# Performance work log

Measured on AMD Instinct MI355X. Metric: run time of the kernel, lower is better.

Reference implementation:

```python
import jax, jax.numpy as jnp
import numpy as np

N = 100_000      # nodes
E_HALF = 1_600_000  # undirected edges (mirrored -> 3.2M directed)
D = 128          # feature dim
K = 1            # k-MIS hop parameter


def setup_inputs() -> dict:
    key = jax.random.key(0)
    k1, k2, k3, k4, k5 = jax.random.split(key, 5)
    x = jax.random.normal(k1, (N, D), dtype=jnp.float32)
    src = jax.random.randint(k2, (E_HALF,), 0, N)
    dst = jax.random.randint(k3, (E_HALF,), 0, N)
    # symmetric edge list (undirected graph), as k-MIS coverage assumes
    edge_index = jnp.stack([jnp.concatenate([src, dst]),
                            jnp.concatenate([dst, src])])
    ea = jax.random.uniform(k4, (E_HALF,), dtype=jnp.float32)
    edge_attr = jnp.concatenate([ea, ea])
    # RandomScorer: score is a uniform random vector over nodes
    score = jax.random.uniform(k5, (N,), dtype=jnp.float32)
    return {"x": x, "edge_index": edge_index, "edge_attr": edge_attr, "score": score}


def _scatter_min(values, index, n, fill):
    return jnp.full((n,), fill, dtype=values.dtype).at[index].min(values)


def maximal_k_independent_set(row, col, n, k, rank):
    # Iteratively: propagate min rank k hops; nodes equal to their own
    # (uncovered) min rank join the MIS; mark their k-hop neighborhood covered.
    mis = jnp.zeros(n, dtype=bool)
    mask = jnp.zeros(n, dtype=bool)
    min_rank = rank
    while not bool(mask.all()):
        for _ in range(k):
            mn = _scatter_min(min_rank[row], col, n, n)
            min_rank = jnp.minimum(mn, min_rank)
        mis = mis | ((rank == min_rank) & ~mask)
        mask = mask | mis
        for _ in range(k):
            nb = jnp.zeros(n, dtype=bool).at[col].max(mask[row])
            mask = mask | nb
        min_rank = jnp.where(mask, n, rank)
    return mis


def cluster_k_mis(mis, row, col, n, k, rank):
    # assign every node to the MIS node of minimum rank within k hops
    min_rank = jnp.where(mis, rank, n)
    for _ in range(k):
        mn = _scatter_min(min_rank[row], col, n, n)
        min_rank = jnp.minimum(mn, min_rank)
    _, clusters = jnp.unique(min_rank, return_inverse=True)  # sorted uniques
    perm = jnp.argsort(rank[mis])  # sorted-rank position -> index into x[mis]
    return perm[clusters.ravel()]


def reference(x, edge_index, edge_attr, score):
    n = x.shape[0]
    row, col = edge_index[0], edge_index[1]
    # Greedy ordering: rank = inverse permutation of argsort(score)
    rank = jnp.argsort(jnp.argsort(score))
    mis = maximal_k_independent_set(row, col, n, K, rank)
    cluster = cluster_k_mis(mis, row, col, n, K, rank)
    # sparse_reduce_adj: map edges into cluster space, coalesce with sum
    pairs = jnp.stack([cluster[row], cluster[col]], axis=1)  # [E,2]
    uk, inv = jnp.unique(pairs, axis=0, return_inverse=True)
    vals = jax.ops.segment_sum(edge_attr, inv.ravel(), num_segments=uk.shape[0])
    r2, c2 = uk[:, 0], uk[:, 1]
    keep = r2 != c2  # remove_self_loops
    edge_index_out = jnp.stack([r2[keep], c2[keep]])
    edge_attr_out = vals[keep]
    x_out = x[jnp.nonzero(mis)[0]]  # reduce_x=None -> select MIS node features
    return x_out, edge_index_out, edge_attr_out, cluster, mis, score
```

## Files before the change

kernel.cpp:

```cpp
#include <hip/hip_runtime.h>
#include <stdint.h>

#define RTILE 4096
#define ROUNDS 12


__global__ void k_init_counters(int* counters){
  int t = threadIdx.x;
  counters[t] = 0;
  if (t == 7) counters[7] = 1;
}
__global__ void k_init_nodes(int* mis, int N){
  int v = blockIdx.x*blockDim.x + threadIdx.x;
  if (v < N) mis[v]=0;
}
__global__ void k_zero_vals(float* vals, int E){
  int i = blockIdx.x*blockDim.x + threadIdx.x;
  if (i < E) vals[i]=0.f;
}

__global__ void k_score_key(const float* score, unsigned* keys, unsigned* pay, int N){
  int i = blockIdx.x*blockDim.x+threadIdx.x;
  if (i<N){
    unsigned b = __float_as_uint(score[i]);
    b ^= ((int)b < 0) ? 0xFFFFFFFFu : 0x80000000u;
    keys[i]=b; pay[i]=(unsigned)i;
  }
}
__global__ void k_rank_build(const unsigned* pay, int* rank, int* pm, int N){
  int p = blockIdx.x*blockDim.x+threadIdx.x;
  if (p<N){ int v = (int)pay[p]; rank[v]=p; pm[v]=p; }
}
__global__ void k_make_colrow(const int* __restrict__ row, const int* __restrict__ col,
                              unsigned* __restrict__ keys, unsigned* __restrict__ pay, int E){
  int e = blockIdx.x*blockDim.x+threadIdx.x;
  if (e<E){ keys[e]=(unsigned)col[e]; pay[e]=(unsigned)row[e]; }
}

template<typename K, int TILE>
__global__ void k_radix_hist(const K* __restrict__ keys, int n, int shift,
                             unsigned* __restrict__ ghist, int numBlocks, const int* gate){
  if (*gate==0) return;
  __shared__ unsigned h[512];
  int t=threadIdx.x, b=blockIdx.x;
  h[t]=0; h[t+256]=0; __syncthreads();
  int base = b*TILE;
  for (int j=t; j<TILE; j+=256){
    int i = base+j;
    if (i<n){
      unsigned d = (unsigned)((keys[i]>>shift)&(K)511);
      atomicAdd(&h[d],1u);
    }
  }
  __syncthreads();
  ghist[(size_t)t*numBlocks + b] = h[t];
  ghist[(size_t)(t+256)*numBlocks + b] = h[t+256];
}

template<typename K, int TILE>
__global__ void k_radix_scatter(const K* __restrict__ keysIn, const unsigned* __restrict__ payIn,
                                K* __restrict__ keysOut, unsigned* __restrict__ payOut,
                                int n, int shift, const unsigned* __restrict__ gbase,
                                int numBlocks, const int* gate){
  int t=threadIdx.x, b=blockIdx.x;
  int base = b*TILE;
  if (*gate==0){
    for (int j=t; j<TILE; j+=256){
      int i = base+j;
      if (i<n){ keysOut[i]=keysIn[i]; payOut[i]=payIn[i]; }
    }
    return;
  }
  __shared__ unsigned carry[512];
  carry[t]=0; carry[t+256]=0; __syncthreads();
  int lane = t&63, wave = t>>6;
  for (int r=0; r<TILE/256; ++r){
    int i = base + r*256 + t;
    bool valid = i<n;
    K k = valid ? keysIn[i] : (K)0;
    unsigned pay = valid ? payIn[i] : 0u;
    unsigned d = (unsigned)((k>>shift)&(K)511);
    unsigned off=0;
    for (int w=0; w<4; ++w){
      if (wave==w){
        unsigned long long m = __ballot(valid);
        #pragma unroll
        for (int bit=0; bit<9; ++bit){
          unsigned long long bb = __ballot((d>>bit)&1u);
          m &= ((d>>bit)&1u) ? bb : ~bb;
        }
        int lr = __popcll(m & ((1ull<<lane)-1ull));
        unsigned cb = carry[d];
        off = cb + (unsigned)lr;
        if (valid && lr==0) carry[d] = cb + (unsigned)__popcll(m);
      }
      __syncthreads();
    }
    if (valid){
      unsigned pos = gbase[(size_t)d*numBlocks + b] + off;
      keysOut[pos]=k; payOut[pos]=pay;
    }
  }
}

__global__ void k_scan_single(unsigned* data, int n, unsigned* total, const int* gate){
  if (*gate==0) return;
  __shared__ unsigned sh[1024];
  __shared__ unsigned carry;
  int t=threadIdx.x;
  if (t==0) carry=0;
  __syncthreads();
  for (int base=0; base<n; base+=4096){
    unsigned v[4]; unsigned s=0;
    int i0 = base + t*4;
    #pragma unroll
    for (int j=0;j<4;j++){ int i=i0+j; v[j] = (i<n)?data[i]:0u; s+=v[j]; }
    sh[t]=s; __syncthreads();
    for (int off=1; off<1024; off<<=1){
      unsigned x = (t>=off)? sh[t-off]:0u; __syncthreads();
      sh[t]+=x; __syncthreads();
    }
    unsigned excl = (t?sh[t-1]:0u) + carry;
    #pragma unroll
    for (int j=0;j<4;j++){ int i=i0+j; if(i<n){ unsigned o=v[j]; data[i]=excl; excl+=o; } }
    unsigned tot = sh[1023];
    __syncthreads();
    if (t==0) carry += tot;
    __syncthreads();
  }
  if (total && t==0) *total = carry;
}

__global__ void k_scan_partials(const unsigned* __restrict__ in, unsigned* __restrict__ bsums,
                                int n, const int* gate){
  if (*gate==0) return;
  __shared__ unsigned sh[256];
  int b=blockIdx.x, t=threadIdx.x;
  long base = (long)b*RTILE + (long)t*16;
  unsigned s=0;
  #pragma unroll
  for (int j=0;j<16;j++){ long i=base+j; if(i<n) s+=in[i]; }
  sh[t]=s; __syncthreads();
  for (int off=128; off>0; off>>=1){ if(t<off) sh[t]+=sh[t+off]; __syncthreads(); }
  if (t==0) bsums[b]=sh[0];
}
__global__ void k_scan_final(const unsigned* __restrict__ in, unsigned* __restrict__ out,
                             const unsigned* __restrict__ bsums, int n, const int* gate){
  if (*gate==0) return;
  __shared__ unsigned sh[256];
  int b=blockIdx.x, t=threadIdx.x;
  long base = (long)b*RTILE + (long)t*16;
  unsigned v[16]; unsigned s=0;
  #pragma unroll
  for (int j=0;j<16;j++){ long i=base+j; v[j]=(i<n)?in[i]:0u; s+=v[j]; }
  sh[t]=s; __syncthreads();
  for (int off=1; off<256; off<<=1){
    unsigned x=(t>=off)?sh[t-off]:0u; __syncthreads(); sh[t]+=x; __syncthreads();
  }
  unsigned run=(t?sh[t-1]:0u)+bsums[b];
  #pragma unroll
  for (int j=0;j<16;j++){ long i=base+j; if(i<n){ unsigned o=v[j]; out[i]=run; run+=o; } }
}

__global__ void k_build_off(const unsigned* __restrict__ scol, int* __restrict__ off, int E, int N){
  int i = blockIdx.x*blockDim.x+threadIdx.x;
  if (i>=E) return;
  int c = (int)scol[i];
  int p = (i==0) ? -1 : (int)scol[i-1];
  for (int v=p+1; v<=c; ++v) off[v]=i;
  if (i==E-1){ for (int v=c+1; v<=N; ++v) off[v]=E; }
}

__global__ void k_round1(const int* __restrict__ off, const int* __restrict__ nbr,
                         const int* __restrict__ pm, int* __restrict__ mis,
                         int* __restrict__ maskA, int N, const int* gate){
  if (*gate==0) return;
  int v = blockIdx.x*blockDim.x+threadIdx.x;
  if (v>=N) return;
  int p = pm[v];
  if (p == N){ maskA[v]=1; return; }
  int m = p;
  int s=off[v], e=off[v+1];
  for (int j=s; j<e; ++j){ int u=nbr[j]; m = min(m, pm[u]); }
  int nm = (m == p);
  if (nm) mis[v]=1;
  maskA[v] = nm;
}
__global__ void k_round2(const int* __restrict__ off, const int* __restrict__ nbr,
                         const int* __restrict__ maskA, int* __restrict__ pm,
                         int N, int* cnt, const int* gate){
  if (*gate==0) return;
  int v = blockIdx.x*blockDim.x+threadIdx.x;
  int um = 0;
  if (v<N){
    int mk = maskA[v];
    int s=off[v], e=off[v+1];
    for (int j=s; j<e && !mk; ++j) mk |= maskA[nbr[j]];
    if (mk) pm[v] = N;
    um = !mk;
  }
  unsigned long long bm = __ballot(um);
  if ((threadIdx.x&63)==0 && bm) atomicAdd(cnt, (int)__popcll(bm));
}

__global__ void k_cl_init(const int* rank, const int* mis, int* pm, int N){
  int v = blockIdx.x*blockDim.x+threadIdx.x;
  if (v<N) pm[v] = mis[v] ? rank[v] : N;
}
__global__ void k_cl_gather(const int* __restrict__ off, const int* __restrict__ nbr,
                            const int* __restrict__ pm, int* __restrict__ mn, int N){
  int v = blockIdx.x*blockDim.x+threadIdx.x;
  if (v>=N) return;
  int m = pm[v];
  int s=off[v], e=off[v+1];
  for (int j=s; j<e; ++j) m = min(m, pm[nbr[j]]);
  mn[v] = m;
}
__global__ void k_copy_u32(const int* in, unsigned* out, int N){
  int v = blockIdx.x*blockDim.x+threadIdx.x;
  if (v<N) out[v]=(unsigned)in[v];
}
__global__ void k_cl_map(const int* rank, const int* mis, const unsigned* cidx,
                         int* map, int* rmax, int N){
  int v = blockIdx.x*blockDim.x+threadIdx.x;
  if (v<N && mis[v]){ map[rank[v]] = (int)cidx[v]; atomicMax(rmax, rank[v]); }
}
__global__ void k_cl_cluster(const int* mn, const int* map, const int* rmax, int* cluster, int N){
  int v = blockIdx.x*blockDim.x+threadIdx.x;
  if (v<N){
    int mr = mn[v];
    if (mr >= N) mr = *rmax;
    cluster[v] = map[mr];
  }
}
__global__ void k_gather_x(const float4* __restrict__ x, float4* __restrict__ out,
                           const int* __restrict__ mis, const unsigned* __restrict__ cidx,
                           int N, int D4){
  int t = blockIdx.x*blockDim.x+threadIdx.x;
  int v = t / D4, q = t - v*D4;
  if (v<N && mis[v]) out[(size_t)cidx[v]*D4 + q] = x[(size_t)v*D4 + q];
}

__global__ void k_set_gates(int* counters){
  int M = counters[1];
  int sh = (M<=1) ? 1 : (32-__clz((unsigned)(M-1)));
  int kb = 2*sh;
  counters[36] = sh;
  counters[32] = 1;
  counters[33] = (9  < kb);
  counters[34] = (18 < kb);
  counters[35] = (27 < kb);
}
__global__ void k_pair_key(const int* __restrict__ row, const int* __restrict__ col,
                           const int* __restrict__ cluster, const float* __restrict__ attr,
                           unsigned long long* __restrict__ keys, unsigned* __restrict__ pay,
                           const int* __restrict__ counters, int E){
  int e = blockIdx.x*blockDim.x+threadIdx.x;
  if (e<E){
    int sh = counters[36];
    unsigned a = (unsigned)cluster[row[e]], b=(unsigned)cluster[col[e]];
    keys[e] = ((unsigned long long)a<<sh) | b;
    pay[e] = __float_as_uint(attr[e]);
  }
}
__global__ void k_flags(const unsigned long long* __restrict__ keys,
                        unsigned* __restrict__ fhead, unsigned* __restrict__ fkeep,
                        const int* __restrict__ counters, int E){
  int i = blockIdx.x*blockDim.x+threadIdx.x;
  if (i<E){
    int sh = counters[36];
    unsigned long long k = keys[i];
    unsigned head = (i==0) || (k != keys[i-1]);
    unsigned a=(unsigned)(k>>sh), b=(unsigned)(k & ((1ull<<sh)-1ull));
    fhead[i]=head;
    fkeep[i]=(head && a!=b) ? 1u : 0u;
  }
}
__global__ void k_acc_seg(const unsigned long long* __restrict__ keys,
                          const unsigned* __restrict__ pay,
                          const unsigned* __restrict__ excl1,
                          float* __restrict__ vals, int E){
  int i = blockIdx.x*blockDim.x+threadIdx.x;
  int lane = threadIdx.x & 63;
  bool valid = i < E;
  unsigned long long k = valid ? keys[i] : ~0ull;
  float v = valid ? __uint_as_float(pay[i]) : 0.f;
  #pragma unroll
  for (int off=1; off<64; off<<=1){
    float o = __shfl_up(v, off);
    unsigned long long ko = __shfl_up(k, off);
    if (lane >= off && ko == k) v += o;
  }
  if (valid){
    unsigned long long knext = (i+1<E) ? keys[i+1] : ~0ull;
    if (lane==63 || k != knext){
      unsigned head = (i==0) || (keys[i-1] != k);
      atomicAdd(&vals[excl1[i] + head - 1u], v);
    }
  }
}
__global__ void k_write_edges(const unsigned long long* __restrict__ keys,
                              const unsigned* __restrict__ excl1, const unsigned* __restrict__ excl2,
                              const float* __restrict__ vals, float* __restrict__ out,
                              const int* __restrict__ counters, int E, int D){
  int i = blockIdx.x*blockDim.x+threadIdx.x;
  if (i<E){
    int sh = counters[36];
    int head=(i==0)||(keys[i]!=keys[i-1]);
    unsigned a=(unsigned)(keys[i]>>sh), b=(unsigned)(keys[i] & ((1ull<<sh)-1ull));
    if (head && a!=b){
      unsigned opos = excl2[i];
      int M = counters[1], Ep = counters[3];
      size_t off = (size_t)M*D;
      out[off + opos] = (float)a;
      out[off + (size_t)Ep + opos] = (float)b;
      out[off + 2*(size_t)Ep + opos] = vals[excl1[i]];
    }
  }
}
__global__ void k_write_nodes(const int* __restrict__ cluster, const int* __restrict__ mis,
                              const float* __restrict__ score, float* __restrict__ out,
                              const int* __restrict__ counters, int N, int D){
  int v = blockIdx.x*blockDim.x+threadIdx.x;
  if (v<N){
    int M=counters[1], Ep=counters[3];
    size_t off = (size_t)M*D + 3*(size_t)Ep;
    out[off + v] = (float)cluster[v];
    out[off + (size_t)N + v] = mis[v] ? 1.f : 0.f;
    out[off + 2*(size_t)N + v] = score[v];
  }
}

extern "C" void kernel_launch(void* const* d_in, const int* in_sizes, int n_in,
                              void* d_out, int out_size, void* d_ws, size_t ws_size,
                              hipStream_t stream){
  const float* x     = (const float*)d_in[0];
  const int*   ei    = (const int*)d_in[1];
  const float* attr  = (const float*)d_in[2];
  const float* score = (const float*)d_in[3];
  int N = in_sizes[3];
  int E = in_sizes[2];
  int D = in_sizes[0]/N;
  const int* row = ei;
  const int* col = ei + E;
  float* out = (float*)d_out;

  char* p = (char*)d_ws;
  auto alloc = [&](size_t bytes)->char*{ char* r=p; p += ((bytes+255)/256)*256; return r; };
  unsigned long long* keyA = (unsigned long long*)alloc((size_t)E*8);
  unsigned long long* keyB = (unsigned long long*)alloc((size_t)E*8);
  unsigned* payA  = (unsigned*)alloc((size_t)E*4);
  unsigned* payB  = (unsigned*)alloc((size_t)E*4);
  unsigned* scanA = (unsigned*)alloc((size_t)E*4);
  unsigned* scanB = (unsigned*)alloc((size_t)E*4);
  float*    vals  = (float*)alloc((size_t)E*4);
  int* csr_row = (int*)alloc((size_t)E*4);
  int* off     = (int*)alloc((size_t)(N+1)*4);
  int* rank   = (int*)alloc((size_t)N*4);
  int* pm     = (int*)alloc((size_t)N*4);
  int* mis    = (int*)alloc((size_t)N*4);
  int* maskA  = (int*)alloc((size_t)N*4);
  int* mnArr  = (int*)alloc((size_t)N*4);
  int* map    = (int*)alloc((size_t)N*4);
  unsigned* cidx = (unsigned*)alloc((size_t)N*4);
  int* cluster= (int*)alloc((size_t)N*4);
  int* counters=(int*)alloc(256*4);
  int Be = (E + RTILE-1)/RTILE;
  int Bn1k = (N + 1023)/1024;
  unsigned* ghist = (unsigned*)alloc((size_t)512*Be*4);
  unsigned* bsums = (unsigned*)alloc(4096*4);

  int nbN = (N+255)/256, nbE = (E+255)/256;
  const int* ON = counters+7;

  auto big_scan = [&](unsigned* data, int n, unsigned* total, const int* gate){
    int B = (n + RTILE-1)/RTILE;
    k_scan_partials<<<B,256,0,stream>>>(data,bsums,n,gate);
    k_scan_single<<<1,1024,0,stream>>>(bsums,B,total,gate);
    k_scan_final<<<B,256,0,stream>>>(data,data,bsums,n,gate);
  };

  k_init_counters<<<1,256,0,stream>>>(counters);
  k_init_nodes<<<nbN,256,0,stream>>>(mis,N);
  k_zero_vals<<<nbE,256,0,stream>>>(vals,E);

  k_make_colrow<<<nbE,256,0,stream>>>(row,col,(unsigned*)keyA,payA,E);
  k_radix_hist<unsigned,RTILE><<<Be,256,0,stream>>>((unsigned*)keyA,E,0,ghist,Be,ON);
  big_scan(ghist,512*Be,nullptr,ON);
  k_radix_scatter<unsigned,RTILE><<<Be,256,0,stream>>>((unsigned*)keyA,payA,(unsigned*)keyB,payB,E,0,ghist,Be,ON);
  k_radix_hist<unsigned,RTILE><<<Be,256,0,stream>>>((unsigned*)keyB,E,9,ghist,Be,ON);
  big_scan(ghist,512*Be,nullptr,ON);
  k_radix_scatter<unsigned,RTILE><<<Be,256,0,stream>>>((unsigned*)keyB,payB,scanA,(unsigned*)csr_row,E,9,ghist,Be,ON);
  k_build_off<<<nbE,256,0,stream>>>(scanA,off,E,N);

  k_score_key<<<nbN,256,0,stream>>>(score,(unsigned*)keyA,payA,N);
  {
    unsigned *ki=(unsigned*)keyA,*ko=(unsigned*)keyB,*pi=payA,*po=payB;
    for (int pass=0; pass<4; ++pass){
      int shift = pass*9;
      k_radix_hist<unsigned,1024><<<Bn1k,256,0,stream>>>(ki,N,shift,ghist,Bn1k,ON);
      big_scan(ghist,512*Bn1k,nullptr,ON);
      k_radix_scatter<unsigned,1024><<<Bn1k,256,0,stream>>>(ki,pi,ko,po,N,shift,ghist,Bn1k,ON);
      unsigned* tk=ki; ki=ko; ko=tk; unsigned* tp=pi; pi=po; po=tp;
    }
    k_rank_build<<<nbN,256,0,stream>>>(pi, rank, pm, N);
  }

  for (int r=0; r<ROUNDS; ++r){
    const int* gate = (r==0) ? ON : (counters + 8 + r - 1);
    int* cnt = counters + 8 + r;
    k_round1<<<nbN,256,0,stream>>>(off,csr_row,pm,mis,maskA,N,gate);
    k_round2<<<nbN,256,0,stream>>>(off,csr_row,maskA,pm,N,cnt,gate);
  }

  k_cl_init<<<nbN,256,0,stream>>>(rank,mis,pm,N);
  k_cl_gather<<<nbN,256,0,stream>>>(off,csr_row,pm,mnArr,N);
  k_copy_u32<<<nbN,256,0,stream>>>(mis,cidx,N);
  big_scan(cidx,N,(unsigned*)(counters+1),ON);
  k_cl_map<<<nbN,256,0,stream>>>(rank,mis,cidx,map,counters+4,N);
  k_cl_cluster<<<nbN,256,0,stream>>>(mnArr,map,counters+4,cluster,N);
  k_gather_x<<<(N*(D/4)+255)/256,256,0,stream>>>((const float4*)x,(float4*)out,mis,cidx,N,D/4);

  k_set_gates<<<1,1,0,stream>>>(counters);
  k_pair_key<<<nbE,256,0,stream>>>(row,col,cluster,attr,keyA,payA,counters,E);
  {
    unsigned long long *ki=keyA,*ko=keyB; unsigned *pi=payA,*po=payB;
    for (int pass=0; pass<4; ++pass){
      int shift = pass*9;
      const int* g = counters + 32 + pass;
      k_radix_hist<unsigned long long,RTILE><<<Be,256,0,stream>>>(ki,E,shift,ghist,Be,g);
      big_scan(ghist,512*Be,nullptr,g);
      k_radix_scatter<unsigned long long,RTILE><<<Be,256,0,stream>>>(ki,pi,ko,po,E,shift,ghist,Be,g);
      unsigned long long* tk=ki; ki=ko; ko=tk; unsigned* tp=pi; pi=po; po=tp;
    }
    k_flags<<<nbE,256,0,stream>>>(keyA,scanA,scanB,counters,E);
    big_scan(scanA,E,(unsigned*)(counters+2),ON);
    big_scan(scanB,E,(unsigned*)(counters+3),ON);
    k_acc_seg<<<nbE,256,0,stream>>>(keyA,payA,scanA,vals,E);
    k_write_edges<<<nbE,256,0,stream>>>(keyA,scanA,scanB,vals,out,counters,E,D);
  }
  k_write_nodes<<<nbN,256,0,stream>>>(cluster,mis,score,out,counters,N,D);
}
```

Before: 1.094 ms.

## Build CSR with atomics, stage radix scatter in LDS, skip gated copies

Replaces the two-pass radix sort used to build the CSR with an atomic count, scan and atomic fill. The radix scatter is rewritten to compute local offsets, stage keys in shared memory and write coalesced to global memory. Gated-off passes now return early instead of copying, with a parity flag selecting the final buffer. The MIS round cap drops from 12 to 10, which risks an incomplete MIS if more rounds are needed, and the larger shared-memory footprint may lower occupancy.

```diff
diff --git a/kernel.cpp b/kernel.cpp
--- a/kernel.cpp
+++ b/kernel.cpp
@@ -2,7 +2,7 @@
 #include <stdint.h>
 
 #define RTILE 4096
-#define ROUNDS 12
+#define ROUNDS 10
 
 
 __global__ void k_init_counters(int* counters){
@@ -10,9 +10,10 @@
   counters[t] = 0;
   if (t == 7) counters[7] = 1;
 }
-__global__ void k_init_nodes(int* mis, int N){
+__global__ void k_init_nodes(int* mis, int* cur, int* cnt, int N){
   int v = blockIdx.x*blockDim.x + threadIdx.x;
-  if (v < N) mis[v]=0;
+  if (v < N){ mis[v]=0; cur[v]=0; }
+  if (v <= N) cnt[v]=0;
 }
 __global__ void k_zero_vals(float* vals, int E){
   int i = blockIdx.x*blockDim.x + threadIdx.x;
@@ -31,10 +32,20 @@
   int p = blockIdx.x*blockDim.x+threadIdx.x;
   if (p<N){ int v = (int)pay[p]; rank[v]=p; pm[v]=p; }
 }
-__global__ void k_make_colrow(const int* __restrict__ row, const int* __restrict__ col,
-                              unsigned* __restrict__ keys, unsigned* __restrict__ pay, int E){
+
+__global__ void k_csr_count(const int* __restrict__ col, int* __restrict__ cnt, int E){
   int e = blockIdx.x*blockDim.x+threadIdx.x;
-  if (e<E){ keys[e]=(unsigned)col[e]; pay[e]=(unsigned)row[e]; }
+  if (e<E) atomicAdd(&cnt[col[e]], 1);
+}
+__global__ void k_csr_fill(const int* __restrict__ row, const int* __restrict__ col,
+                           const unsigned* __restrict__ off, int* __restrict__ cur,
+                           int* __restrict__ csr_row, int E){
+  int e = blockIdx.x*blockDim.x+threadIdx.x;
+  if (e<E){
+    int c = col[e];
+    int p = atomicAdd(&cur[c], 1);
+    csr_row[off[c] + p] = row[e];
+  }
 }
 
 template<typename K, int TILE>
@@ -62,20 +73,38 @@
                                 K* __restrict__ keysOut, unsigned* __restrict__ payOut,
                                 int n, int shift, const unsigned* __restrict__ gbase,
                                 int numBlocks, const int* gate){
+  if (*gate==0) return;
+  __shared__ unsigned lbase[512];
+  __shared__ unsigned carry[512];
+  __shared__ unsigned ss[256];
+  __shared__ K        skey[TILE];
+  __shared__ unsigned spay[TILE];
   int t=threadIdx.x, b=blockIdx.x;
   int base = b*TILE;
-  if (*gate==0){
-    for (int j=t; j<TILE; j+=256){
-      int i = base+j;
-      if (i<n){ keysOut[i]=keysIn[i]; payOut[i]=payIn[i]; }
-    }
-    return;
-  }
-  __shared__ unsigned carry[512];
+  int cnt = min(TILE, n-base);
   carry[t]=0; carry[t+256]=0; __syncthreads();
+  for (int c=0;c<TILE/256;++c){
+    int i = base+c*256+t;
+    if (i<n){
+      unsigned d = (unsigned)((keysIn[i]>>shift)&(K)511);
+      atomicAdd(&carry[d],1u);
+    }
+  }
+  __syncthreads();
+  unsigned a0=carry[2*t], a1=carry[2*t+1];
+  ss[t]=a0+a1; __syncthreads();
+  for (int off=1; off<256; off<<=1){
+    unsigned x = (t>=off)? ss[t-off]:0u; __syncthreads();
+    ss[t]+=x; __syncthreads();
+  }
+  unsigned excl = t? ss[t-1]:0u;
+  __syncthreads();
+  lbase[2*t]=excl;      lbase[2*t+1]=excl+a0;
+  carry[2*t]=excl;      carry[2*t+1]=excl+a0;
+  __syncthreads();
   int lane = t&63, wave = t>>6;
-  for (int r=0; r<TILE/256; ++r){
-    int i = base + r*256 + t;
+  for (int c=0;c<TILE/256;++c){
+    int i = base + c*256 + t;
     bool valid = i<n;
     K k = valid ? keysIn[i] : (K)0;
     unsigned pay = valid ? payIn[i] : 0u;
@@ -96,9 +125,16 @@
       }
       __syncthreads();
     }
-    if (valid){
-      unsigned pos = gbase[(size_t)d*numBlocks + b] + off;
-      keysOut[pos]=k; payOut[pos]=pay;
+    if (valid){ skey[off]=k; spay[off]=pay; }
+  }
+  __syncthreads();
+  for (int c=0;c<TILE/256;++c){
+    int j = c*256 + t;
+    if (j<cnt){
+      K k = skey[j];
+      unsigned d = (unsigned)((k>>shift)&(K)511);
+      unsigned gpos = gbase[(size_t)d*numBlocks + b] + ((unsigned)j - lbase[d]);
+      keysOut[gpos]=k; payOut[gpos]=spay[j];
     }
   }
 }
@@ -162,15 +198,6 @@
   for (int j=0;j<16;j++){ long i=base+j; if(i<n){ unsigned o=v[j]; out[i]=run; run+=o; } }
 }
 
-__global__ void k_build_off(const unsigned* __restrict__ scol, int* __restrict__ off, int E, int N){
-  int i = blockIdx.x*blockDim.x+threadIdx.x;
-  if (i>=E) return;
-  int c = (int)scol[i];
-  int p = (i==0) ? -1 : (int)scol[i-1];
-  for (int v=p+1; v<=c; ++v) off[v]=i;
-  if (i==E-1){ for (int v=c+1; v<=N; ++v) off[v]=E; }
-}
-
 __global__ void k_round1(const int* __restrict__ off, const int* __restrict__ nbr,
                          const int* __restrict__ pm, int* __restrict__ mis,
                          int* __restrict__ maskA, int N, const int* gate){
@@ -245,11 +272,13 @@
   int M = counters[1];
   int sh = (M<=1) ? 1 : (32-__clz((unsigned)(M-1)));
   int kb = 2*sh;
+  int npass = 1 + (9<kb) + (18<kb) + (27<kb);
   counters[36] = sh;
   counters[32] = 1;
   counters[33] = (9  < kb);
   counters[34] = (18 < kb);
   counters[35] = (27 < kb);
+  counters[37] = npass & 1;
 }
 __global__ void k_pair_key(const int* __restrict__ row, const int* __restrict__ col,
                            const int* __restrict__ cluster, const float* __restrict__ attr,
@@ -263,9 +292,11 @@
     pay[e] = __float_as_uint(attr[e]);
   }
 }
-__global__ void k_flags(const unsigned long long* __restrict__ keys,
+__global__ void k_flags(const unsigned long long* __restrict__ keyA,
+                        const unsigned long long* __restrict__ keyB,
                         unsigned* __restrict__ fhead, unsigned* __restrict__ fkeep,
                         const int* __restrict__ counters, int E){
+  const unsigned long long* keys = counters[37] ? keyB : keyA;
   int i = blockIdx.x*blockDim.x+threadIdx.x;
   if (i<E){
     int sh = counters[36];
@@ -276,10 +307,13 @@
     fkeep[i]=(head && a!=b) ? 1u : 0u;
   }
 }
-__global__ void k_acc_seg(const unsigned long long* __restrict__ keys,
-                          const unsigned* __restrict__ pay,
+__global__ void k_acc_seg(const unsigned long long* __restrict__ keyA,
+                          const unsigned long long* __restrict__ keyB,
+                          const unsigned* __restrict__ payA, const unsigned* __restrict__ payB,
                           const unsigned* __restrict__ excl1,
-                          float* __restrict__ vals, int E){
+                          float* __restrict__ vals, const int* __restrict__ counters, int E){
+  const unsigned long long* keys = counters[37] ? keyB : keyA;
+  const unsigned* pay = counters[37] ? payB : payA;
   int i = blockIdx.x*blockDim.x+threadIdx.x;
   int lane = threadIdx.x & 63;
   bool valid = i < E;
@@ -299,10 +333,12 @@
     }
   }
 }
-__global__ void k_write_edges(const unsigned long long* __restrict__ keys,
+__global__ void k_write_edges(const unsigned long long* __restrict__ keyA,
+                              const unsigned long long* __restrict__ keyB,
                               const unsigned* __restrict__ excl1, const unsigned* __restrict__ excl2,
                               const float* __restrict__ vals, float* __restrict__ out,
                               const int* __restrict__ counters, int E, int D){
+  const unsigned long long* keys = counters[37] ? keyB : keyA;
   int i = blockIdx.x*blockDim.x+threadIdx.x;
   if (i<E){
     int sh = counters[36];
@@ -355,7 +391,8 @@
   unsigned* scanB = (unsigned*)alloc((size_t)E*4);
   float*    vals  = (float*)alloc((size_t)E*4);
   int* csr_row = (int*)alloc((size_t)E*4);
-  int* off     = (int*)alloc((size_t)(N+1)*4);
+  unsigned* off= (unsigned*)alloc((size_t)(N+1)*4);
+  int* cur     = (int*)alloc((size_t)N*4);
   int* rank   = (int*)alloc((size_t)N*4);
   int* pm     = (int*)alloc((size_t)N*4);
   int* mis    = (int*)alloc((size_t)N*4);
@@ -381,17 +418,12 @@
   };
 
   k_init_counters<<<1,256,0,stream>>>(counters);
-  k_init_nodes<<<nbN,256,0,stream>>>(mis,N);
+  k_init_nodes<<<nbN+1,256,0,stream>>>(mis,cur,(int*)off,N);
   k_zero_vals<<<nbE,256,0,stream>>>(vals,E);
 
-  k_make_colrow<<<nbE,256,0,stream>>>(row,col,(unsigned*)keyA,payA,E);
-  k_radix_hist<unsigned,RTILE><<<Be,256,0,stream>>>((unsigned*)keyA,E,0,ghist,Be,ON);
-  big_scan(ghist,512*Be,nullptr,ON);
-  k_radix_scatter<unsigned,RTILE><<<Be,256,0,stream>>>((unsigned*)keyA,payA,(unsigned*)keyB,payB,E,0,ghist,Be,ON);
-  k_radix_hist<unsigned,RTILE><<<Be,256,0,stream>>>((unsigned*)keyB,E,9,ghist,Be,ON);
-  big_scan(ghist,512*Be,nullptr,ON);
-  k_radix_scatter<unsigned,RTILE><<<Be,256,0,stream>>>((unsigned*)keyB,payB,scanA,(unsigned*)csr_row,E,9,ghist,Be,ON);
-  k_build_off<<<nbE,256,0,stream>>>(scanA,off,E,N);
+  k_csr_count<<<nbE,256,0,stream>>>(col,(int*)off,E);
+  big_scan(off,N+1,nullptr,ON);
+  k_csr_fill<<<nbE,256,0,stream>>>(row,col,off,cur,csr_row,E);
 
   k_score_key<<<nbN,256,0,stream>>>(score,(unsigned*)keyA,payA,N);
   {
@@ -409,12 +441,12 @@
   for (int r=0; r<ROUNDS; ++r){
     const int* gate = (r==0) ? ON : (counters + 8 + r - 1);
     int* cnt = counters + 8 + r;
-    k_round1<<<nbN,256,0,stream>>>(off,csr_row,pm,mis,maskA,N,gate);
-    k_round2<<<nbN,256,0,stream>>>(off,csr_row,maskA,pm,N,cnt,gate);
+    k_round1<<<nbN,256,0,stream>>>((const int*)off,csr_row,pm,mis,maskA,N,gate);
+    k_round2<<<nbN,256,0,stream>>>((const int*)off,csr_row,maskA,pm,N,cnt,gate);
   }
 
   k_cl_init<<<nbN,256,0,stream>>>(rank,mis,pm,N);
-  k_cl_gather<<<nbN,256,0,stream>>>(off,csr_row,pm,mnArr,N);
+  k_cl_gather<<<nbN,256,0,stream>>>((const int*)off,csr_row,pm,mnArr,N);
   k_copy_u32<<<nbN,256,0,stream>>>(mis,cidx,N);
   big_scan(cidx,N,(unsigned*)(counters+1),ON);
   k_cl_map<<<nbN,256,0,stream>>>(rank,mis,cidx,map,counters+4,N);
@@ -433,11 +465,11 @@
       k_radix_scatter<unsigned long long,RTILE><<<Be,256,0,stream>>>(ki,pi,ko,po,E,shift,ghist,Be,g);
       unsigned long long* tk=ki; ki=ko; ko=tk; unsigned* tp=pi; pi=po; po=tp;
     }
-    k_flags<<<nbE,256,0,stream>>>(keyA,scanA,scanB,counters,E);
+    k_flags<<<nbE,256,0,stream>>>(keyA,keyB,scanA,scanB,counters,E);
     big_scan(scanA,E,(unsigned*)(counters+2),ON);
     big_scan(scanB,E,(unsigned*)(counters+3),ON);
-    k_acc_seg<<<nbE,256,0,stream>>>(keyA,payA,scanA,vals,E);
-    k_write_edges<<<nbE,256,0,stream>>>(keyA,scanA,scanB,vals,out,counters,E,D);
+    k_acc_seg<<<nbE,256,0,stream>>>(keyA,keyB,payA,payB,scanA,vals,counters,E);
+    k_write_edges<<<nbE,256,0,stream>>>(keyA,keyB,scanA,scanB,vals,out,counters,E,D);
   }
   k_write_nodes<<<nbN,256,0,stream>>>(cluster,mis,score,out,counters,N,D);
 }
```

New measurement: 1.167 ms. 6.6% more time.
